# Kernel optimization log

Measured on AMD Instinct MI355X. Metric: run time of the kernel, lower is better.

## Reference

```python
import jax, jax.numpy as jnp
import numpy as np

NUM_HOSTS = 13


def gcn_conv_max(x, src, dst, n, W, b):
    """PyG GCNConv with aggr='max': x@W, gcn_norm (self-loops + sym norm), max-scatter, +bias.
    src/dst already include self-loop edges."""
    xw = x @ W  # [N, out]
    deg = jnp.zeros((n,), xw.dtype).at[dst].add(1.0)
    dinv = jax.lax.rsqrt(deg)  # deg >= 1 thanks to self-loops
    norm = dinv[src] * dinv[dst]  # [E+N]
    msg = norm[:, None] * xw[src]  # [E+N, out] -- the big gather
    agg = jax.ops.segment_max(msg, dst, num_segments=n)
    return agg + b


def self_attn(v, g, aW, ab, fW, fb, gW, gb):
    """SimpleSelfAttention: softmax over feature dim, weighted-sum over nodes, residual global update."""
    att = jax.nn.softmax(v @ aW + ab, axis=-1)  # [B, Nh, h]
    feat = v @ fW + fb                            # [B, Nh, h]
    out = jnp.sum(att * feat, axis=1)             # [B, h]
    g_ = jnp.concatenate([out, g], axis=-1) @ gW + gb
    return g + g_


def setup_inputs() -> dict:
    key = jax.random.key(0)
    ks = jax.random.split(key, 24)
    IN, H1, H2 = 64, 256, 64
    B, NPG = 256, 200
    N = B * NPG
    E = 409600

    x = jax.random.normal(ks[0], (N, IN), jnp.float32)
    host_idx = (jnp.arange(B)[:, None] * NPG + jnp.arange(NUM_HOSTS)[None, :]).reshape(-1).astype(jnp.int32)
    x = x.at[host_idx, 0].set(1.0)  # hosts = x[:,0]==1
    ei = jax.random.randint(ks[1], (2, E), 0, N, dtype=jnp.int64)

    def lin(k, i, o):
        k1, k2 = jax.random.split(k)
        s = 1.0 / np.sqrt(i)
        return (jax.random.uniform(k1, (i, o), jnp.float32, -s, s),
                jax.random.uniform(k2, (o,), jnp.float32, -s, s))

    W1, b1 = lin(ks[2], IN, H1)
    W2, b2 = lin(ks[3], H1, H2)
    # g0: in=IN, h=H1, g=H1 ; g1: in=H1, h=H1 ; g2: in=H2, h=H2
    a0W, a0b = lin(ks[4], IN, H1); f0W, f0b = lin(ks[5], IN, H1); g0W, g0b = lin(ks[6], H1 + H1, H1)
    a1W, a1b = lin(ks[7], H1, H1); f1W, f1b = lin(ks[8], H1, H1); g1W, g1b = lin(ks[9], H1 + H1, H1)
    a2W, a2b = lin(ks[10], H2, H2); f2W, f2b = lin(ks[11], H2, H2); g2W, g2b = lin(ks[12], H2 + H1, H1)
    o1W, o1b = lin(ks[13], H1, H2)
    o2W, o2b = lin(ks[14], H2, 1)

    return dict(x=x, ei=ei, host_idx=host_idx,
                W1=W1, b1=b1, W2=W2, b2=b2,
                a0W=a0W, a0b=a0b, f0W=f0W, f0b=f0b, g0W=g0W, g0b=g0b,
                a1W=a1W, a1b=a1b, f1W=f1W, f1b=f1b, g1W=g1W, g1b=g1b,
                a2W=a2W, a2b=a2b, f2W=f2W, f2b=f2b, g2W=g2W, g2b=g2b,
                o1W=o1W, o1b=o1b, o2W=o2W, o2b=o2b)


def reference(x, ei, host_idx,
              W1, b1, W2, b2,
              a0W, a0b, f0W, f0b, g0W, g0b,
              a1W, a1b, f1W, f1b, g1W, g1b,
              a2W, a2b, f2W, f2b, g2W, g2b,
              o1W, o1b, o2W, o2b):
    n = x.shape[0]
    B = host_idx.shape[0] // NUM_HOSTS
    loops = jnp.arange(n, dtype=ei.dtype)
    src = jnp.concatenate([ei[0], loops])
    dst = jnp.concatenate([ei[1], loops])

    hx = x[host_idx].reshape(B, NUM_HOSTS, -1)
    g = self_attn(hx, jnp.zeros((B, g0b.shape[0]), x.dtype), a0W, a0b, f0W, f0b, g0W, g0b)

    x1 = jax.nn.relu(gcn_conv_max(x, src, dst, n, W1, b1))
    g = self_attn(x1[host_idx].reshape(B, NUM_HOSTS, -1), g, a1W, a1b, f1W, f1b, g1W, g1b)

    x2 = jax.nn.relu(gcn_conv_max(x1, src, dst, n, W2, b2))
    g = self_attn(x2[host_idx].reshape(B, NUM_HOSTS, -1), g, a2W, a2b, f2W, f2b, g2W, g2b)

    return jax.nn.relu(g @ o1W + o1b) @ o2W + o2b  # [B, 1]
```

## Files before the change

### kernel.cpp

```cpp
#include <hip/hip_runtime.h>
#include <math.h>
#include <stdio.h>

#define N_NODES 51200
#define N_EDGES 409600
#define B_GRAPH 256
#define NH 13

typedef float v4f __attribute__((ext_vector_type(4)));
typedef unsigned v2u __attribute__((ext_vector_type(2)));
__device__ __forceinline__ void nt_store_u2(uint2* p, uint2 v) {
    v2u w; w.x = v.x; w.y = v.y;
    __builtin_nontemporal_store(w, (v2u*)p);
}

__device__ __forceinline__ unsigned pack_bf2(float a, float b) {
    unsigned ua = __float_as_uint(a);
    ua = (ua + 0x7fffu + ((ua >> 16) & 1u)) >> 16;
    unsigned ub = __float_as_uint(b);
    ub = (ub + 0x7fffu + ((ub >> 16) & 1u)) & 0xffff0000u;
    return ua | ub;
}
__device__ __forceinline__ float bf_lo(unsigned u) { return __uint_as_float(u << 16); }
__device__ __forceinline__ float bf_hi(unsigned u) { return __uint_as_float(u & 0xffff0000u); }

__device__ __forceinline__ bool ei_is_64(const int* __restrict__ ei32) {
    int z = 1;
    #pragma unroll
    for (int k = 1; k < 16; k += 2) z &= (ei32[k] == 0);
    return z != 0;
}

__global__ void count_deg(const int* __restrict__ ei32, const long long* __restrict__ ei64,
                          int* __restrict__ degc) {
    int e = blockIdx.x * 256 + threadIdx.x;
    if (e >= N_EDGES) return;
    int v = ei_is_64(ei32) ? (int)ei64[N_EDGES + e] : ei32[N_EDGES + e];
    atomicAdd(&degc[v], 1);
}

__global__ void scan_block_sums(const int* __restrict__ degc, int* __restrict__ bsums) {
    __shared__ int sdata[256];
    int i = blockIdx.x * 256 + threadIdx.x;
    sdata[threadIdx.x] = degc[i];
    __syncthreads();
    for (int s = 128; s > 0; s >>= 1) {
        if (threadIdx.x < s) sdata[threadIdx.x] += sdata[threadIdx.x + s];
        __syncthreads();
    }
    if (threadIdx.x == 0) bsums[blockIdx.x] = sdata[0];
}

__global__ void scan_finalize(int* __restrict__ degc, int* __restrict__ offs,
                              float* __restrict__ dinv, const int* __restrict__ bsums) {
    __shared__ int bs[256];
    __shared__ int s[256];
    const int t = threadIdx.x;
    bs[t] = (t < 200) ? bsums[t] : 0;
    __syncthreads();
    for (int off = 1; off < 256; off <<= 1) {
        int u = (t >= off) ? bs[t - off] : 0;
        __syncthreads();
        bs[t] += u;
        __syncthreads();
    }
    int i = blockIdx.x * 256 + t;
    int cnt = degc[i];
    s[t] = cnt;
    __syncthreads();
    for (int off = 1; off < 256; off <<= 1) {
        int u = (t >= off) ? s[t - off] : 0;
        __syncthreads();
        s[t] += u;
        __syncthreads();
    }
    int base = (blockIdx.x == 0) ? 0 : bs[blockIdx.x - 1];
    int excl = base + s[t] - cnt;
    offs[i] = excl;
    dinv[i] = rsqrtf((float)(cnt + 1));
    degc[i] = excl;
    if (i == N_NODES - 1) offs[N_NODES] = N_EDGES;
}

template <int K, int WS, bool BF16IN>
__device__ __forceinline__ void gemm_body64(const float* __restrict__ X,
        const float* __restrict__ W, const float* __restrict__ bias,
        float* __restrict__ Y, int row0, const int* __restrict__ rows,
        float* __restrict__ xs, float* __restrict__ ws) {
    constexpr int BK = 32;
    constexpr int XS = BK + 4;
    const int t = threadIdx.x;
    const int ct = t & 15;
    const int rt = t >> 4;
    float acc[4][4] = {{0.f}};
    for (int kc = 0; kc < K; kc += BK) {
        __syncthreads();
        #pragma unroll
        for (int i = 0; i < 2; ++i) {
            int idx = t + i * 256;
            int q = idx & 7, r = idx >> 3;
            int xr = rows[r];
            float4 v;
            if (BF16IN) {
                uint2 pv = ((const uint2*)X)[(size_t)xr * (K / 4) + kc / 4 + q];
                v = make_float4(bf_lo(pv.x), bf_hi(pv.x), bf_lo(pv.y), bf_hi(pv.y));
            } else {
                v = *(const float4*)(X + (size_t)xr * K + kc + q * 4);
            }
            *(float4*)&xs[r * XS + q * 4] = v;
        }
        #pragma unroll
        for (int i = 0; i < 2; ++i) {
            int idx = t + i * 256;
            int q = idx & 15, k = idx >> 4;
            float4 v = *(const float4*)(W + (size_t)(kc + k) * WS + q * 4);
            *(float4*)&ws[k * 64 + q * 4] = v;
        }
        __syncthreads();
        #pragma unroll
        for (int kb = 0; kb < BK; kb += 4) {
            float4 wv[4];
            #pragma unroll
            for (int kk = 0; kk < 4; ++kk)
                wv[kk] = *(const float4*)&ws[(kb + kk) * 64 + ct * 4];
            #pragma unroll
            for (int r = 0; r < 4; ++r) {
                float4 xv = *(const float4*)&xs[(rt * 4 + r) * XS + kb];
                float xk[4] = {xv.x, xv.y, xv.z, xv.w};
                #pragma unroll
                for (int kk = 0; kk < 4; ++kk) {
                    acc[r][0] = fmaf(xk[kk], wv[kk].x, acc[r][0]);
                    acc[r][1] = fmaf(xk[kk], wv[kk].y, acc[r][1]);
                    acc[r][2] = fmaf(xk[kk], wv[kk].z, acc[r][2]);
                    acc[r][3] = fmaf(xk[kk], wv[kk].w, acc[r][3]);
                }
            }
        }
    }
    #pragma unroll
    for (int r = 0; r < 4; ++r) {
        int row = row0 + rt * 4 + r;
        float4 o = make_float4(acc[r][0] + bias[ct * 4 + 0],
                               acc[r][1] + bias[ct * 4 + 1],
                               acc[r][2] + bias[ct * 4 + 2],
                               acc[r][3] + bias[ct * 4 + 3]);
        *(float4*)&Y[(size_t)row * 512 + ct * 4] = o;
    }
}

template <int K, int WS, int YS, int NCOLB, int CPT, bool BF16IN, bool BF16OUT>
__device__ __forceinline__ void gemm_main(const float* __restrict__ X,
        const float* __restrict__ W, const float* __restrict__ dinv,
        float* __restrict__ Y, int row0,
        float* __restrict__ xs, float* __restrict__ ws) {
    constexpr int BK = 32;
    constexpr int XS = BK + 4;
    constexpr int CQ = CPT / 4;
    const int t = threadIdx.x;
    const int ct = t & 15;
    const int rt = t >> 4;
    float acc[8][CPT];
    #pragma unroll
    for (int r = 0; r < 8; ++r)
        #pragma unroll
        for (int c = 0; c < CPT; ++c) acc[r][c] = 0.f;
    for (int kc = 0; kc < K; kc += BK) {
        __syncthreads();
        #pragma unroll
        for (int i = 0; i < 4; ++i) {
            int idx = t + i * 256;
            int q = idx & 7, r = idx >> 3;
            float4 v;
            if (BF16IN) {
                uint2 pv = ((const uint2*)X)[(size_t)(row0 + r) * (K / 4) + kc / 4 + q];
                v = make_float4(bf_lo(pv.x), bf_hi(pv.x), bf_lo(pv.y), bf_hi(pv.y));
            } else {
                v = *(const float4*)(X + (size_t)(row0 + r) * K + kc + q * 4);
            }
            *(float4*)&xs[r * XS + q * 4] = v;
        }
        #pragma unroll
        for (int i = 0; i < NCOLB / 32; ++i) {
            int idx = t + i * 256;
            int q = idx & (NCOLB / 4 - 1), k = idx / (NCOLB / 4);
            float4 v = *(const float4*)(W + (size_t)(kc + k) * WS + q * 4);
            *(float4*)&ws[k * NCOLB + q * 4] = v;
        }
        __syncthreads();
        #pragma unroll
        for (int kb = 0; kb < BK; kb += 4) {
            float4 wv[4][CQ];
            #pragma unroll
            for (int kk = 0; kk < 4; ++kk)
                #pragma unroll
                for (int cq = 0; cq < CQ; ++cq)
                    wv[kk][cq] = *(const float4*)&ws[(kb + kk) * NCOLB + cq * 64 + ct * 4];
            #pragma unroll
            for (int r = 0; r < 8; ++r) {
                float4 xv = *(const float4*)&xs[(rt + 16 * r) * XS + kb];
                float xk[4] = {xv.x, xv.y, xv.z, xv.w};
                #pragma unroll
                for (int kk = 0; kk < 4; ++kk)
                    #pragma unroll
                    for (int cq = 0; cq < CQ; ++cq) {
                        acc[r][cq * 4 + 0] = fmaf(xk[kk], wv[kk][cq].x, acc[r][cq * 4 + 0]);
                        acc[r][cq * 4 + 1] = fmaf(xk[kk], wv[kk][cq].y, acc[r][cq * 4 + 1]);
                        acc[r][cq * 4 + 2] = fmaf(xk[kk], wv[kk][cq].z, acc[r][cq * 4 + 2]);
                        acc[r][cq * 4 + 3] = fmaf(xk[kk], wv[kk][cq].w, acc[r][cq * 4 + 3]);
                    }
            }
        }
    }
    #pragma unroll
    for (int r = 0; r < 8; ++r) {
        int row = row0 + rt + 16 * r;
        float sc = dinv[row];
        #pragma unroll
        for (int cq = 0; cq < CQ; ++cq) {
            float4 o = make_float4(acc[r][cq * 4 + 0] * sc, acc[r][cq * 4 + 1] * sc,
                                   acc[r][cq * 4 + 2] * sc, acc[r][cq * 4 + 3] * sc);
            if (BF16OUT) {
                unsigned short* yb = (unsigned short*)Y + (size_t)row * YS;
                uint2 pk;
                pk.x = pack_bf2(o.x, o.y);
                pk.y = pack_bf2(o.z, o.w);
                ((uint2*)yb)[cq * 16 + ct] = pk;
            } else {
                *(float4*)&Y[(size_t)row * YS + cq * 64 + ct * 4] = o;
            }
        }
    }
}

__global__ __launch_bounds__(256) void fused_gemm1(const float* __restrict__ x,
        const float* __restrict__ W1, float* __restrict__ xw1b,
        const float* __restrict__ dinv,
        const int* __restrict__ ei32, const long long* __restrict__ ei64,
        int* __restrict__ cursor, int* __restrict__ csr,
        const int* __restrict__ host_idx,
        const float* __restrict__ a0W, const float* __restrict__ a0b,
        const float* __restrict__ f0W, const float* __restrict__ f0b,
        float* __restrict__ AF) {
    __shared__ float xs[128 * 36];
    __shared__ float ws[32 * 128];
    __shared__ int rows[64];
    const int bid = blockIdx.x;
    const int t = threadIdx.x;
    if (bid < 416) {
        const int rb = bid >> 3;
        const int cb = bid & 7;
        const int c0 = cb * 64;
        const float* Wp = (c0 < 256) ? (a0W + c0) : (f0W + (c0 - 256));
        const float* bp = (c0 < 256) ? (a0b + c0) : (f0b + (c0 - 256));
        if (t < 64) rows[t] = host_idx[rb * 64 + t];
        __syncthreads();
        gemm_body64<64, 256, false>(x, Wp, bp, AF + c0, rb * 64, rows, xs, ws);
    } else if (bid < 2016) {
        int e = (bid - 416) * 256 + t;
        if (e < N_EDGES) {
            int u, v;
            if (ei_is_64(ei32)) { u = (int)ei64[e]; v = (int)ei64[N_EDGES + e]; }
            else                { u = ei32[e];      v = ei32[N_EDGES + e]; }
            int pos = atomicAdd(&cursor[v], 1);
            csr[pos] = u;
        }
    } else {
        const int gbid = bid - 2016;
        const int rb = gbid >> 1;
        const int cb = gbid & 1;
        gemm_main<64, 256, 256, 128, 8, false, true>(
            x, W1 + cb * 128, dinv, xw1b + cb * 64, rb * 128, xs, ws);
    }
}

__global__ __launch_bounds__(256) void fused_gemm2(const float* __restrict__ x1b,
        const float* __restrict__ W2, float* __restrict__ xw2,
        const float* __restrict__ dinv,
        const int* __restrict__ host_idx,
        const float* __restrict__ a1W, const float* __restrict__ a1b,
        const float* __restrict__ f1W, const float* __restrict__ f1b,
        float* __restrict__ AF) {
    __shared__ float xs[128 * 36];
    __shared__ float ws[32 * 64];
    __shared__ int rows[64];
    const int bid = blockIdx.x;
    const int t = threadIdx.x;
    if (bid < 416) {
        const int rb = bid >> 3;
        const int cb = bid & 7;
        const int c0 = cb * 64;
        const float* Wp = (c0 < 256) ? (a1W + c0) : (f1W + (c0 - 256));
        const float* bp = (c0 < 256) ? (a1b + c0) : (f1b + (c0 - 256));
        if (t < 64) rows[t] = host_idx[rb * 64 + t];
        __syncthreads();
        gemm_body64<256, 256, true>(x1b, Wp, bp, AF + c0, rb * 64, rows, xs, ws);
    } else {
        const int gbid = bid - 416;
        gemm_main<256, 64, 64, 64, 4, true, false>(
            x1b, W2, dinv, xw2, gbid * 128, xs, ws);
    }
}

__device__ __forceinline__ void attn_red256(const float* __restrict__ AF,
        const float* __restrict__ gW, const float* __restrict__ gb,
        const float* __restrict__ g_in, float* __restrict__ g_out, int b,
        float (*At)[256], float* red_m, float* red_s, float* cat) {
    const int t = threadIdx.x;
    const int wave = t >> 6, lane = t & 63;
    float accA[NH], accF[NH];
    #pragma unroll
    for (int j = 0; j < NH; ++j) {
        const float* r = AF + (size_t)(b * NH + j) * 512;
        accA[j] = r[t];
        accF[j] = r[256 + t];
        At[j][t] = accA[j];
    }
    __syncthreads();
    for (int j = wave; j < NH; j += 4) {
        float m = -3.402823466e38f;
        #pragma unroll
        for (int q = 0; q < 4; ++q) m = fmaxf(m, At[j][q * 64 + lane]);
        #pragma unroll
        for (int off = 32; off; off >>= 1) m = fmaxf(m, __shfl_xor(m, off));
        if (lane == 0) red_m[j] = m;
    }
    __syncthreads();
    #pragma unroll
    for (int j = 0; j < NH; ++j) At[j][t] = expf(accA[j] - red_m[j]);
    __syncthreads();
    for (int j = wave; j < NH; j += 4) {
        float s = 0.f;
        #pragma unroll
        for (int q = 0; q < 4; ++q) s += At[j][q * 64 + lane];
        #pragma unroll
        for (int off = 32; off; off >>= 1) s += __shfl_xor(s, off);
        if (lane == 0) red_s[j] = s;
    }
    __syncthreads();
    float outc = 0.f;
    #pragma unroll
    for (int j = 0; j < NH; ++j) outc += At[j][t] / red_s[j] * accF[j];
    cat[t] = outc;
    float gv = g_in ? g_in[b * 256 + t] : 0.f;
    cat[256 + t] = gv;
    __syncthreads();
    float acc = gb[t];
    const float* gwp = gW + t;
    #pragma unroll 4
    for (int i4 = 0; i4 < 128; ++i4) {
        float4 cq = ((const float4*)cat)[i4];
        const float* gw4 = gwp + (size_t)i4 * 4 * 256;
        acc = fmaf(cq.x, gw4[0], acc);
        acc = fmaf(cq.y, gw4[256], acc);
        acc = fmaf(cq.z, gw4[512], acc);
        acc = fmaf(cq.w, gw4[768], acc);
    }
    g_out[b * 256 + t] = gv + acc;
}

__global__ __launch_bounds__(256) void fused_agg256(const uint2* __restrict__ xwb,
        const float* __restrict__ dinv, const int* __restrict__ offs,
        const int* __restrict__ csr, const float* __restrict__ bias,
        uint2* __restrict__ outb,
        const float* __restrict__ AF, const float* __restrict__ gW,
        const float* __restrict__ gb, const float* __restrict__ g_in,
        float* __restrict__ g_out) {
    __shared__ float At[NH][256];
    __shared__ float red_m[NH];
    __shared__ float red_s[NH];
    __shared__ float cat[512];
    const int bid = blockIdx.x;
    if (bid < 256) {
        attn_red256(AF, gW, gb, g_in, g_out, bid, At, red_m, red_s, cat);
        return;
    }
    int gid = (bid - 256) * 256 + threadIdx.x;
    int v = gid >> 6;
    int lane = gid & 63;
    uint2 sw = xwb[(size_t)v * 64 + lane];
    float4 acc = make_float4(bf_lo(sw.x), bf_hi(sw.x), bf_lo(sw.y), bf_hi(sw.y));
    int e0 = offs[v];
    int e1 = offs[v + 1];
    int em = e0 + ((e1 - e0) & ~7);
    for (int e = e0; e < em; e += 8) {
        int u[8];
        #pragma unroll
        for (int i = 0; i < 8; ++i) u[i] = csr[e + i];
        uint2 m[8];
        #pragma unroll
        for (int i = 0; i < 8; ++i) m[i] = xwb[(size_t)u[i] * 64 + lane];
        #pragma unroll
        for (int i = 0; i < 8; ++i) {
            acc.x = fmaxf(acc.x, bf_lo(m[i].x));
            acc.y = fmaxf(acc.y, bf_hi(m[i].x));
            acc.z = fmaxf(acc.z, bf_lo(m[i].y));
            acc.w = fmaxf(acc.w, bf_hi(m[i].y));
        }
    }
    if (em < e1) {
        int u[8];
        #pragma unroll
        for (int i = 0; i < 8; ++i) u[i] = csr[(em + i < e1) ? (em + i) : (e1 - 1)];
        uint2 m[8];
        #pragma unroll
        for (int i = 0; i < 8; ++i) m[i] = xwb[(size_t)u[i] * 64 + lane];
        #pragma unroll
        for (int i = 0; i < 8; ++i) {
            if (em + i < e1) {
                acc.x = fmaxf(acc.x, bf_lo(m[i].x));
                acc.y = fmaxf(acc.y, bf_hi(m[i].x));
                acc.z = fmaxf(acc.z, bf_lo(m[i].y));
                acc.w = fmaxf(acc.w, bf_hi(m[i].y));
            }
        }
    }
    float dv = dinv[v];
    float4 b4 = ((const float4*)bias)[lane];
    float4 o;
    o.x = fmaxf(fmaf(acc.x, dv, b4.x), 0.f);
    o.y = fmaxf(fmaf(acc.y, dv, b4.y), 0.f);
    o.z = fmaxf(fmaf(acc.z, dv, b4.z), 0.f);
    o.w = fmaxf(fmaf(acc.w, dv, b4.w), 0.f);
    uint2 pk;
    pk.x = pack_bf2(o.x, o.y);
    pk.y = pack_bf2(o.z, o.w);
    nt_store_u2(outb + (size_t)v * 64 + lane, pk);
}

__global__ __launch_bounds__(1024) void attn_graph_head(
        const float* __restrict__ AF,
        const float* __restrict__ g1W, const float* __restrict__ g1b,
        const float* __restrict__ g_in,
        const float* __restrict__ xw2,
        const float* __restrict__ dinv, const int* __restrict__ offs,
        const int* __restrict__ csr, const float* __restrict__ b2,
        const int* __restrict__ host_idx,
        const float* __restrict__ a2W, const float* __restrict__ a2b,
        const float* __restrict__ f2W, const float* __restrict__ f2b,
        const float* __restrict__ g2W, const float* __restrict__ g2b,
        const float* __restrict__ o1W, const float* __restrict__ o1b,
        const float* __restrict__ o2W, const float* __restrict__ o2b,
        float* __restrict__ out) {
    __shared__ float At[NH][256];
    __shared__ float Ft[NH][256];
    __shared__ float red_m[NH];
    __shared__ float red_s[NH];
    __shared__ float cat[512];
    __shared__ float catB[320];
    __shared__ float g1s[256];
    __shared__ float x2l[NH][64];
    __shared__ float part4[4][256];
    __shared__ float part16[16][64];
    __shared__ float grow[256];
    const int b = blockIdx.x;
    const int t = threadIdx.x;
    const int wave = t >> 6;
    const int lane = t & 63;
    const int c = t & 255;
    const int quad = t >> 8;

    if (wave < NH) {
        int hv = host_idx[b * NH + wave];
        float acc = xw2[(size_t)hv * 64 + lane];
        int e0 = offs[hv], e1 = offs[hv + 1];
        for (int e = e0; e < e1; e += 8) {
            int u[8];
            #pragma unroll
            for (int i = 0; i < 8; ++i) u[i] = csr[(e + i < e1) ? (e + i) : (e1 - 1)];
            float m[8];
            #pragma unroll
            for (int i = 0; i < 8; ++i) m[i] = xw2[(size_t)u[i] * 64 + lane];
            #pragma unroll
            for (int i = 0; i < 8; ++i)
                if (e + i < e1) acc = fmaxf(acc, m[i]);
        }
        x2l[wave][lane] = fmaxf(fmaf(acc, dinv[hv], b2[lane]), 0.f);
    }
    for (int idx = t; idx < NH * 128; idx += 1024) {
        int j = idx >> 7, q = idx & 127;
        float4 v = ((const float4*)(AF + (size_t)(b * NH + j) * 512))[q];
        if (q < 64) *(float4*)&At[j][q * 4] = v;
        else        *(float4*)&Ft[j][(q - 64) * 4] = v;
    }
    __syncthreads();
    if (wave < NH) {
        float m = -3.402823466e38f;
        #pragma unroll
        for (int q = 0; q < 4; ++q) m = fmaxf(m, At[wave][q * 64 + lane]);
        #pragma unroll
        for (int off = 32; off; off >>= 1) m = fmaxf(m, __shfl_xor(m, off));
        if (lane == 0) red_m[wave] = m;
    }
    __syncthreads();
    for (int idx = t; idx < NH * 256; idx += 1024) {
        int j = idx >> 8, cc = idx & 255;
        At[j][cc] = expf(At[j][cc] - red_m[j]);
    }
    __syncthreads();
    if (wave < NH) {
        float s = 0.f;
        #pragma unroll
        for (int q = 0; q < 4; ++q) s += At[wave][q * 64 + lane];
        #pragma unroll
        for (int off = 32; off; off >>= 1) s += __shfl_xor(s, off);
        if (lane == 0) red_s[wave] = s;
    }
    __syncthreads();
    if (quad == 0) {
        float outc = 0.f;
        #pragma unroll
        for (int j = 0; j < NH; ++j) outc += At[j][c] / red_s[j] * Ft[j][c];
        cat[c] = outc;
        cat[256 + c] = g_in[b * 256 + c];
    }
    __syncthreads();
    {
        float acc = 0.f;
        const float* gwp = g1W + c;
        #pragma unroll 4
        for (int i4 = quad * 32; i4 < quad * 32 + 32; ++i4) {
            float4 cq = ((const float4*)cat)[i4];
            const float* gw4 = gwp + (size_t)i4 * 1024;
            acc = fmaf(cq.x, gw4[0], acc);
            acc = fmaf(cq.y, gw4[256], acc);
            acc = fmaf(cq.z, gw4[512], acc);
            acc = fmaf(cq.w, gw4[768], acc);
        }
        part4[quad][c] = acc;
    }
    __syncthreads();
    if (quad == 0)
        g1s[c] = cat[256 + c] + g1b[c] +
                 part4[0][c] + part4[1][c] + part4[2][c] + part4[3][c];
    __syncthreads();
    if (wave < NH) {
        float aA = a2b[lane], aF = f2b[lane];
        #pragma unroll 8
        for (int k = 0; k < 64; ++k) {
            float xv = x2l[wave][k];
            aA = fmaf(xv, a2W[k * 64 + lane], aA);
            aF = fmaf(xv, f2W[k * 64 + lane], aF);
        }
        float m = aA;
        #pragma unroll
        for (int off = 32; off; off >>= 1) m = fmaxf(m, __shfl_xor(m, off));
        float pexp = expf(aA - m);
        float s = pexp;
        #pragma unroll
        for (int off = 32; off; off >>= 1) s += __shfl_xor(s, off);
        At[wave][lane] = pexp / s * aF;
    }
    __syncthreads();
    if (t < 64) {
        float o = 0.f;
        #pragma unroll
        for (int j = 0; j < NH; ++j) o += At[j][t];
        catB[t] = o;
    }
    if (quad == 0) catB[64 + c] = g1s[c];
    __syncthreads();
    {
        float acc = 0.f;
        const float* gwp = g2W + c;
        #pragma unroll 4
        for (int i4 = quad * 20; i4 < quad * 20 + 20; ++i4) {
            float4 cq = ((const float4*)catB)[i4];
            const float* gw4 = gwp + (size_t)i4 * 1024;
            acc = fmaf(cq.x, gw4[0], acc);
            acc = fmaf(cq.y, gw4[256], acc);
            acc = fmaf(cq.z, gw4[512], acc);
            acc = fmaf(cq.w, gw4[768], acc);
        }
        part4[quad][c] = acc;
    }
    __syncthreads();
    if (quad == 0)
        grow[c] = g1s[c] + g2b[c] +
                  part4[0][c] + part4[1][c] + part4[2][c] + part4[3][c];
    __syncthreads();
    {
        float hp = 0.f;
        #pragma unroll
        for (int k = wave * 16; k < wave * 16 + 16; ++k)
            hp = fmaf(grow[k], o1W[(size_t)k * 64 + lane], hp);
        part16[wave][lane] = hp;
    }
    __syncthreads();
    if (wave == 0) {
        float h = o1b[lane];
        #pragma unroll
        for (int w = 0; w < 16; ++w) h += part16[w][lane];
        h = fmaxf(h, 0.f);
        float sres = h * o2W[lane];
        #pragma unroll
        for (int off = 32; off; off >>= 1) sres += __shfl_xor(sres, off);
        if (lane == 0) out[b] = sres + o2b[0];
    }
}

extern "C" void kernel_launch(void* const* d_in, const int* in_sizes, int n_in,
                              void* d_out, int out_size, void* d_ws, size_t ws_size,
                              hipStream_t stream) {
    (void)in_sizes; (void)n_in; (void)out_size;
    const float* x    = (const float*)d_in[0];
    const int* ei32   = (const int*)d_in[1];
    const long long* ei64 = (const long long*)d_in[1];
    const int* hidx   = (const int*)d_in[2];
    const float* W1 = (const float*)d_in[3],  *b1 = (const float*)d_in[4];
    const float* W2 = (const float*)d_in[5],  *b2 = (const float*)d_in[6];
    const float* a0W = (const float*)d_in[7],  *a0b = (const float*)d_in[8];
    const float* f0W = (const float*)d_in[9],  *f0b = (const float*)d_in[10];
    const float* g0W = (const float*)d_in[11], *g0b = (const float*)d_in[12];
    const float* a1W = (const float*)d_in[13], *a1b = (const float*)d_in[14];
    const float* f1W = (const float*)d_in[15], *f1b = (const float*)d_in[16];
    const float* g1W = (const float*)d_in[17], *g1b = (const float*)d_in[18];
    const float* a2W = (const float*)d_in[19], *a2b = (const float*)d_in[20];
    const float* f2W = (const float*)d_in[21], *f2b = (const float*)d_in[22];
    const float* g2W = (const float*)d_in[23], *g2b = (const float*)d_in[24];
    const float* o1W = (const float*)d_in[25], *o1b = (const float*)d_in[26];
    const float* o2W = (const float*)d_in[27], *o2b = (const float*)d_in[28];
    float* outp = (float*)d_out;

    char* p = (char*)d_ws;
    auto alloc = [&](size_t bytes) {
        char* r = p;
        p += (bytes + 255) & ~(size_t)255;
        return r;
    };
    float* dinv = (float*)alloc((size_t)N_NODES * 4);
    int* degc   = (int*)alloc((size_t)N_NODES * 4);
    int* offs   = (int*)alloc((size_t)(N_NODES + 1) * 4);
    int* csr    = (int*)alloc((size_t)N_EDGES * 4);
    int* bsums  = (int*)alloc(256 * 4);
    float* g    = (float*)alloc((size_t)B_GRAPH * 256 * 4);
    float* AF   = (float*)alloc((size_t)B_GRAPH * NH * 512 * 4);
    unsigned short* xw1b = (unsigned short*)alloc((size_t)N_NODES * 256 * 2);
    unsigned short* x1b  = (unsigned short*)alloc((size_t)N_NODES * 256 * 2);
    float* xw2  = (float*)alloc((size_t)N_NODES * 64 * 4);

    size_t need = (size_t)(p - (char*)d_ws);
    if (need > ws_size) {
        fprintf(stderr, "kernel_launch: ws too small (%zu needed, %zu have)\n", need, ws_size);
        return;
    }

    (void)hipMemsetAsync(degc, 0, (size_t)N_NODES * 4, stream);
    count_deg<<<1600, 256, 0, stream>>>(ei32, ei64, degc);
    scan_block_sums<<<200, 256, 0, stream>>>(degc, bsums);
    scan_finalize<<<200, 256, 0, stream>>>(degc, offs, dinv, bsums);

    fused_gemm1<<<2816, 256, 0, stream>>>(
        x, W1, (float*)xw1b, dinv, ei32, ei64, degc, csr,
        hidx, a0W, a0b, f0W, f0b, AF);
    fused_agg256<<<256 + 12800, 256, 0, stream>>>((const uint2*)xw1b, dinv, offs, csr,
                                                  b1, (uint2*)x1b, AF, g0W, g0b,
                                                  nullptr, g);
    fused_gemm2<<<816, 256, 0, stream>>>(
        (const float*)x1b, W2, xw2, dinv, hidx, a1W, a1b, f1W, f1b, AF);
    attn_graph_head<<<256, 1024, 0, stream>>>(
        AF, g1W, g1b, g, xw2, dinv, offs, csr, b2, hidx,
        a2W, a2b, f2W, f2b, g2W, g2b, o1W, o1b, o2W, o2b, outp);
}
```

Measured before the change: 300.1 us.

## Use smaller 64x64 tiles for GEMM1 and reorder fused block roles

Adds a 64x64-tile GEMM variant for the x@W1 projection, which raises the block count from 800 large tiles to 3200 small ones and halves shared memory per block. The main GEMM blocks are moved to the front of the block index range in both fused kernels, ahead of the host-attention GEMMs and the CSR fill. The aim is better occupancy and load balance, and getting the heavy work started early. The cost is more redundant loads of X and W per output, since each block covers fewer columns and rows.

```diff
diff --git a/kernel.cpp b/kernel.cpp
--- a/kernel.cpp
+++ b/kernel.cpp
@@ -145,6 +145,72 @@
                                acc[r][2] + bias[ct * 4 + 2],
                                acc[r][3] + bias[ct * 4 + 3]);
         *(float4*)&Y[(size_t)row * 512 + ct * 4] = o;
+    }
+}
+
+template <int K, int WS, int YS, bool BF16OUT>
+__device__ __forceinline__ void gemm_main64(const float* __restrict__ X,
+        const float* __restrict__ W, const float* __restrict__ dinv,
+        float* __restrict__ Y, int row0,
+        float* __restrict__ xs, float* __restrict__ ws) {
+    constexpr int BK = 32;
+    constexpr int XS = BK + 4;
+    const int t = threadIdx.x;
+    const int ct = t & 15;
+    const int rt = t >> 4;
+    float acc[4][4] = {{0.f}};
+    for (int kc = 0; kc < K; kc += BK) {
+        __syncthreads();
+        #pragma unroll
+        for (int i = 0; i < 2; ++i) {
+            int idx = t + i * 256;
+            int q = idx & 7, r = idx >> 3;
+            float4 v = *(const float4*)(X + (size_t)(row0 + r) * K + kc + q * 4);
+            *(float4*)&xs[r * XS + q * 4] = v;
+        }
+        #pragma unroll
+        for (int i = 0; i < 2; ++i) {
+            int idx = t + i * 256;
+            int q = idx & 15, k = idx >> 4;
+            float4 v = *(const float4*)(W + (size_t)(kc + k) * WS + q * 4);
+            *(float4*)&ws[k * 64 + q * 4] = v;
+        }
+        __syncthreads();
+        #pragma unroll
+        for (int kb = 0; kb < BK; kb += 4) {
+            float4 wv[4];
+            #pragma unroll
+            for (int kk = 0; kk < 4; ++kk)
+                wv[kk] = *(const float4*)&ws[(kb + kk) * 64 + ct * 4];
+            #pragma unroll
+            for (int r = 0; r < 4; ++r) {
+                float4 xv = *(const float4*)&xs[(rt * 4 + r) * XS + kb];
+                float xk[4] = {xv.x, xv.y, xv.z, xv.w};
+                #pragma unroll
+                for (int kk = 0; kk < 4; ++kk) {
+                    acc[r][0] = fmaf(xk[kk], wv[kk].x, acc[r][0]);
+                    acc[r][1] = fmaf(xk[kk], wv[kk].y, acc[r][1]);
+                    acc[r][2] = fmaf(xk[kk], wv[kk].z, acc[r][2]);
+                    acc[r][3] = fmaf(xk[kk], wv[kk].w, acc[r][3]);
+                }
+            }
+        }
+    }
+    #pragma unroll
+    for (int r = 0; r < 4; ++r) {
+        int row = row0 + rt * 4 + r;
+        float sc = dinv[row];
+        float4 o = make_float4(acc[r][0] * sc, acc[r][1] * sc,
+                               acc[r][2] * sc, acc[r][3] * sc);
+        if (BF16OUT) {
+            unsigned short* yb = (unsigned short*)Y + (size_t)row * YS;
+            uint2 pk;
+            pk.x = pack_bf2(o.x, o.y);
+            pk.y = pack_bf2(o.z, o.w);
+            ((uint2*)yb)[ct] = pk;
+        } else {
+            *(float4*)&Y[(size_t)row * YS + ct * 4] = o;
+        }
     }
 }
 
@@ -241,22 +307,28 @@
         const float* __restrict__ a0W, const float* __restrict__ a0b,
         const float* __restrict__ f0W, const float* __restrict__ f0b,
         float* __restrict__ AF) {
-    __shared__ float xs[128 * 36];
-    __shared__ float ws[32 * 128];
+    __shared__ float xs[64 * 36];
+    __shared__ float ws[32 * 64];
     __shared__ int rows[64];
     const int bid = blockIdx.x;
     const int t = threadIdx.x;
-    if (bid < 416) {
-        const int rb = bid >> 3;
-        const int cb = bid & 7;
+    if (bid < 3200) {
+        const int rb = bid >> 2;
+        const int cb = bid & 3;
+        gemm_main64<64, 256, 256, true>(
+            x, W1 + cb * 64, dinv, xw1b + cb * 32, rb * 64, xs, ws);
+    } else if (bid < 3616) {
+        const int abid = bid - 3200;
+        const int rb = abid >> 3;
+        const int cb = abid & 7;
         const int c0 = cb * 64;
         const float* Wp = (c0 < 256) ? (a0W + c0) : (f0W + (c0 - 256));
         const float* bp = (c0 < 256) ? (a0b + c0) : (f0b + (c0 - 256));
         if (t < 64) rows[t] = host_idx[rb * 64 + t];
         __syncthreads();
         gemm_body64<64, 256, false>(x, Wp, bp, AF + c0, rb * 64, rows, xs, ws);
-    } else if (bid < 2016) {
-        int e = (bid - 416) * 256 + t;
+    } else {
+        int e = (bid - 3616) * 256 + t;
         if (e < N_EDGES) {
             int u, v;
             if (ei_is_64(ei32)) { u = (int)ei64[e]; v = (int)ei64[N_EDGES + e]; }
@@ -264,12 +336,6 @@
             int pos = atomicAdd(&cursor[v], 1);
             csr[pos] = u;
         }
-    } else {
-        const int gbid = bid - 2016;
-        const int rb = gbid >> 1;
-        const int cb = gbid & 1;
-        gemm_main<64, 256, 256, 128, 8, false, true>(
-            x, W1 + cb * 128, dinv, xw1b + cb * 64, rb * 128, xs, ws);
     }
 }
 
@@ -285,19 +351,19 @@
     __shared__ int rows[64];
     const int bid = blockIdx.x;
     const int t = threadIdx.x;
-    if (bid < 416) {
-        const int rb = bid >> 3;
-        const int cb = bid & 7;
+    if (bid < 400) {
+        gemm_main<256, 64, 64, 64, 4, true, false>(
+            x1b, W2, dinv, xw2, bid * 128, xs, ws);
+    } else {
+        const int abid = bid - 400;
+        const int rb = abid >> 3;
+        const int cb = abid & 7;
         const int c0 = cb * 64;
         const float* Wp = (c0 < 256) ? (a1W + c0) : (f1W + (c0 - 256));
         const float* bp = (c0 < 256) ? (a1b + c0) : (f1b + (c0 - 256));
         if (t < 64) rows[t] = host_idx[rb * 64 + t];
         __syncthreads();
         gemm_body64<256, 256, true>(x1b, Wp, bp, AF + c0, rb * 64, rows, xs, ws);
-    } else {
-        const int gbid = bid - 416;
-        gemm_main<256, 64, 64, 64, 4, true, false>(
-            x1b, W2, dinv, xw2, gbid * 128, xs, ws);
     }
 }
 
@@ -649,7 +715,7 @@
     scan_block_sums<<<200, 256, 0, stream>>>(degc, bsums);
     scan_finalize<<<200, 256, 0, stream>>>(degc, offs, dinv, bsums);
 
-    fused_gemm1<<<2816, 256, 0, stream>>>(
+    fused_gemm1<<<5216, 256, 0, stream>>>(
         x, W1, (float*)xw1b, dinv, ei32, ei64, degc, csr,
         hidx, a0W, a0b, f0W, f0b, AF);
     fused_agg256<<<256 + 12800, 256, 0, stream>>>((const uint2*)xw1b, dinv, offs, csr,
```

Result: faster. 282.4 us (-5.9%).
